# Performance work log

Measured on AMD Instinct MI355X. Metric: run time of the kernel, lower is better.

Reference implementation:

```python
import jax, jax.numpy as jnp
import numpy as np

D_MODEL = 1024
NUM_HEADS = 16
HEAD_DIM = D_MODEL // NUM_HEADS


def setup_inputs() -> dict:
    key = jax.random.key(0)
    k_x, k_wqkv, k_bqkv, k_wfc, k_bfc = jax.random.split(key, 5)
    scale_in = 1.0 / np.sqrt(D_MODEL)
    return {
        "x": jax.random.normal(k_x, (2, 2048, D_MODEL), dtype=jnp.float32),
        # torch nn.Linear stores weight as [out_features, in_features]
        "w_qkv": jax.random.uniform(k_wqkv, (3 * D_MODEL, D_MODEL), jnp.float32, -scale_in, scale_in),
        "b_qkv": jax.random.uniform(k_bqkv, (3 * D_MODEL,), jnp.float32, -scale_in, scale_in),
        "w_fc": jax.random.uniform(k_wfc, (D_MODEL, D_MODEL), jnp.float32, -scale_in, scale_in),
        "b_fc": jax.random.uniform(k_bfc, (D_MODEL,), jnp.float32, -scale_in, scale_in),
    }


def reference(x, w_qkv, b_qkv, w_fc, b_fc):
    B, S, _ = x.shape
    # fused QKV projection: [B,S,3*d_model]
    qkv = jnp.einsum("bsd,ed->bse", x, w_qkv) + b_qkv
    # [B,S,H,3*head_dim] -> [B,H,S,3*head_dim]
    qkv = qkv.reshape(B, S, NUM_HEADS, 3 * HEAD_DIM).transpose(0, 2, 1, 3)
    Q, K, V = jnp.split(qkv, 3, axis=-1)  # each [B,H,S,head_dim]
    scores = jnp.einsum("bhqd,bhkd->bhqk", Q, K) / np.sqrt(HEAD_DIM).astype(np.float32)
    attention = jax.nn.softmax(scores, axis=-1)  # [B,H,S,S]
    values = jnp.einsum("bhqk,bhkd->bhqd", attention, V)
    # [B,H,S,head_dim] -> [B,S,d_model]
    values = values.transpose(0, 2, 1, 3).reshape(B, S, D_MODEL)
    out = jnp.einsum("bsd,ed->bse", values, w_fc) + b_fc
    return out
```

## Files before the change

kernel.cpp:

```cpp
#include <hip/hip_runtime.h>
#include <hip/hip_bf16.h>

#define D_MODEL 1024
#define NH 16
#define HD 64
#define BATCH 2
#define SEQ 2048

typedef __attribute__((ext_vector_type(8))) short short8;
typedef __attribute__((ext_vector_type(4))) float floatx4;

static __device__ __forceinline__ short f2bf(float f) {
    __hip_bfloat16 h = __float2bfloat16(f);
    return *reinterpret_cast<short*>(&h);
}

__global__ __launch_bounds__(256) void cvt_all(
    const float* __restrict__ x, const float* __restrict__ wq,
    const float* __restrict__ wf,
    short* __restrict__ Xb, short* __restrict__ Wqb, short* __restrict__ Wfb)
{
    int i = blockIdx.x * 256 + threadIdx.x;
    const float* src; short* dst; int off;
    if (i < 524288)      { src = x;  dst = Xb;  off = i; }
    else if (i < 917504) { src = wq; dst = Wqb; off = i - 524288; }
    else                 { src = wf; dst = Wfb; off = i - 917504; }
    float4 a = *reinterpret_cast<const float4*>(src + off * 8);
    float4 b = *reinterpret_cast<const float4*>(src + off * 8 + 4);
    short8 o;
    o[0] = f2bf(a.x); o[1] = f2bf(a.y); o[2] = f2bf(a.z); o[3] = f2bf(a.w);
    o[4] = f2bf(b.x); o[5] = f2bf(b.y); o[6] = f2bf(b.z); o[7] = f2bf(b.w);
    *reinterpret_cast<short8*>(dst + off * 8) = o;
}

__global__ __launch_bounds__(256) void qkv_gemm(
    const short* __restrict__ X, const short* __restrict__ W,
    const float* __restrict__ bias,
    short* __restrict__ Qs, short* __restrict__ Ks, short* __restrict__ Vt_g)
{
    __shared__ __align__(16) short As[128][72];
    __shared__ __align__(16) short Bs[128][72];
    const int tid = threadIdx.x;
    const int m0 = blockIdx.y * 128;
    const int n0 = blockIdx.x * 128;
    const int w = tid >> 6, lane = tid & 63;
    const int quad = lane >> 4, l15 = lane & 15;
    const int wm = (w >> 1) * 64, wn = (w & 1) * 64;

    floatx4 acc[4][4];
#pragma unroll
    for (int i = 0; i < 4; i++)
#pragma unroll
        for (int j = 0; j < 4; j++) acc[i][j] = (floatx4)0.0f;

    for (int k0 = 0; k0 < 1024; k0 += 64) {
        __syncthreads();
#pragma unroll
        for (int i = 0; i < 4; i++) {
            int c = tid + i * 256;
            int row = c >> 3, ck = c & 7;
            *reinterpret_cast<uint4*>(&As[row][ck * 8]) =
                *reinterpret_cast<const uint4*>(&X[(m0 + row) * 1024 + k0 + ck * 8]);
            *reinterpret_cast<uint4*>(&Bs[row][ck * 8]) =
                *reinterpret_cast<const uint4*>(&W[(n0 + row) * 1024 + k0 + ck * 8]);
        }
        __syncthreads();
#pragma unroll
        for (int kk = 0; kk < 2; kk++) {
            short8 a[4], b[4];
#pragma unroll
            for (int t = 0; t < 4; t++) {
                a[t] = *reinterpret_cast<const short8*>(&As[wm + t * 16 + l15][kk * 32 + quad * 8]);
                b[t] = *reinterpret_cast<const short8*>(&Bs[wn + t * 16 + l15][kk * 32 + quad * 8]);
            }
#pragma unroll
            for (int mt = 0; mt < 4; mt++)
#pragma unroll
                for (int nt = 0; nt < 4; nt++)
                    acc[mt][nt] = __builtin_amdgcn_mfma_f32_16x16x32_bf16(
                        a[mt], b[nt], acc[mt][nt], 0, 0, 0);
        }
    }

#pragma unroll
    for (int nt = 0; nt < 4; nt++) {
        int col = n0 + wn + nt * 16 + l15;
        float bv = bias[col];
        int h = col / 192;
        int j = col - h * 192;
#pragma unroll
        for (int mt = 0; mt < 4; mt++) {
#pragma unroll
            for (int r = 0; r < 4; r++) {
                int row = m0 + wm + mt * 16 + quad * 4 + r;
                float v = acc[mt][nt][r] + bv;
                int bi = row >> 11, s = row & 2047;
                int bh = bi * NH + h;
                if (j < 64)       Qs[(bh * SEQ + s) * HD + j] = f2bf(v * 0.125f);
                else if (j < 128) Ks[(bh * SEQ + s) * HD + (j - 64)] = f2bf(v);
                else              Vt_g[(bh * HD + (j - 128)) * SEQ + s] = f2bf(v);
            }
        }
    }
}

__global__ __launch_bounds__(256) void attn_kernel(
    const short* __restrict__ Qs, const short* __restrict__ Ks,
    const short* __restrict__ Vt_g, short* __restrict__ attn)
{
    __shared__ __align__(16) char smem[2 * 64 * 72 * 2];
    __shared__ __align__(16) short Pl[4][32][40];
    __shared__ float Ls[64];

    short (*Kl)[72] = (short(*)[72])smem;
    short (*Vt)[72] = (short(*)[72])(smem + 64 * 72 * 2);
    float (*Osum)[66] = (float(*)[66])smem;

    const int tid = threadIdx.x;
    const int w = tid >> 6, lane = tid & 63;
    const int wq = w >> 1, wk = w & 1;
    const int quad = lane >> 4, l15 = lane & 15;
    const int q0 = blockIdx.x * 64;
    const int h = blockIdx.y, bi = blockIdx.z;
    const int bh = bi * NH + h;
    const int kbase = bh * SEQ * HD;
    const int vbase = bh * HD * SEQ;

    short8 aq[2][2];
#pragma unroll
    for (int mt = 0; mt < 2; mt++) {
        const short* qp = Qs + kbase + (q0 + wq * 32 + mt * 16 + l15) * HD;
#pragma unroll
        for (int c = 0; c < 2; c++)
            aq[mt][c] = *reinterpret_cast<const short8*>(qp + c * 32 + quad * 8);
    }

    float l_acc[2][4];
    floatx4 o[2][4];
#pragma unroll
    for (int mt = 0; mt < 2; mt++) {
#pragma unroll
        for (int r = 0; r < 4; r++) l_acc[mt][r] = 0.f;
#pragma unroll
        for (int nt = 0; nt < 4; nt++) o[mt][nt] = (floatx4)0.0f;
    }

    for (int kt = 0; kt < SEQ; kt += 64) {
        __syncthreads();
#pragma unroll
        for (int i = 0; i < 2; i++) {
            int c = tid + i * 256;
            int row = c >> 3, ck = c & 7;
            *reinterpret_cast<uint4*>(&Kl[row][ck * 8]) =
                *reinterpret_cast<const uint4*>(&Ks[kbase + (kt + row) * HD + ck * 8]);
            *reinterpret_cast<uint4*>(&Vt[row][ck * 8]) =
                *reinterpret_cast<const uint4*>(&Vt_g[vbase + row * SEQ + kt + ck * 8]);
        }
        __syncthreads();

        floatx4 sf[2][2];
#pragma unroll
        for (int mt = 0; mt < 2; mt++)
#pragma unroll
            for (int nt = 0; nt < 2; nt++) sf[mt][nt] = (floatx4)0.0f;
#pragma unroll
        for (int c = 0; c < 2; c++) {
#pragma unroll
            for (int nt = 0; nt < 2; nt++) {
                short8 bk = *reinterpret_cast<const short8*>(
                    &Kl[wk * 32 + nt * 16 + l15][c * 32 + quad * 8]);
#pragma unroll
                for (int mt = 0; mt < 2; mt++)
                    sf[mt][nt] = __builtin_amdgcn_mfma_f32_16x16x32_bf16(
                        aq[mt][c], bk, sf[mt][nt], 0, 0, 0);
            }
        }

#pragma unroll
        for (int mt = 0; mt < 2; mt++) {
#pragma unroll
            for (int nt = 0; nt < 2; nt++) {
#pragma unroll
                for (int r = 0; r < 4; r++) {
                    float e = __expf(sf[mt][nt][r]);
                    l_acc[mt][r] += e;
                    Pl[w][mt * 16 + quad * 4 + r][nt * 16 + l15] = f2bf(e);
                }
            }
        }
        asm volatile("s_waitcnt lgkmcnt(0)" ::: "memory");

#pragma unroll
        for (int mt = 0; mt < 2; mt++) {
            short8 ap = *reinterpret_cast<const short8*>(&Pl[w][mt * 16 + l15][quad * 8]);
#pragma unroll
            for (int nt = 0; nt < 4; nt++) {
                short8 bv = *reinterpret_cast<const short8*>(
                    &Vt[nt * 16 + l15][wk * 32 + quad * 8]);
                o[mt][nt] = __builtin_amdgcn_mfma_f32_16x16x32_bf16(
                    ap, bv, o[mt][nt], 0, 0, 0);
            }
        }
    }

#pragma unroll
    for (int mt = 0; mt < 2; mt++)
#pragma unroll
        for (int r = 0; r < 4; r++)
#pragma unroll
            for (int mask = 1; mask < 16; mask <<= 1)
                l_acc[mt][r] += __shfl_xor(l_acc[mt][r], mask);

    __syncthreads();
    if (wk == 0) {
#pragma unroll
        for (int mt = 0; mt < 2; mt++) {
#pragma unroll
            for (int nt = 0; nt < 4; nt++)
#pragma unroll
                for (int r = 0; r < 4; r++)
                    Osum[wq * 32 + mt * 16 + quad * 4 + r][nt * 16 + l15] = o[mt][nt][r];
            if (l15 == 0)
#pragma unroll
                for (int r = 0; r < 4; r++)
                    Ls[wq * 32 + mt * 16 + quad * 4 + r] = l_acc[mt][r];
        }
    }
    __syncthreads();
    if (wk == 1) {
#pragma unroll
        for (int mt = 0; mt < 2; mt++) {
#pragma unroll
            for (int r = 0; r < 4; r++) {
                int qrow = wq * 32 + mt * 16 + quad * 4 + r;
                float lt = Ls[qrow] + l_acc[mt][r];
#pragma unroll
                for (int nt = 0; nt < 4; nt++) {
                    float val = (o[mt][nt][r] + Osum[qrow][nt * 16 + l15]) / lt;
                    attn[(bi * SEQ + q0 + qrow) * D_MODEL + h * HD + nt * 16 + l15] = f2bf(val);
                }
            }
        }
    }
}

__global__ __launch_bounds__(256) void fc_gemm(
    const short* __restrict__ A, const short* __restrict__ W,
    const float* __restrict__ bias, float* __restrict__ out)
{
    __shared__ __align__(16) short As[128][72];
    __shared__ __align__(16) short Bs[128][72];
    const int tid = threadIdx.x;
    const int m0 = blockIdx.y * 128;
    const int n0 = blockIdx.x * 128;
    const int w = tid >> 6, lane = tid & 63;
    const int quad = lane >> 4, l15 = lane & 15;
    const int wm = (w >> 1) * 64, wn = (w & 1) * 64;

    floatx4 acc[4][4];
#pragma unroll
    for (int i = 0; i < 4; i++)
#pragma unroll
        for (int j = 0; j < 4; j++) acc[i][j] = (floatx4)0.0f;

    for (int k0 = 0; k0 < 1024; k0 += 64) {
        __syncthreads();
#pragma unroll
        for (int i = 0; i < 4; i++) {
            int c = tid + i * 256;
            int row = c >> 3, ck = c & 7;
            *reinterpret_cast<uint4*>(&As[row][ck * 8]) =
                *reinterpret_cast<const uint4*>(&A[(m0 + row) * 1024 + k0 + ck * 8]);
            *reinterpret_cast<uint4*>(&Bs[row][ck * 8]) =
                *reinterpret_cast<const uint4*>(&W[(n0 + row) * 1024 + k0 + ck * 8]);
        }
        __syncthreads();
#pragma unroll
        for (int kk = 0; kk < 2; kk++) {
            short8 a[4], b[4];
#pragma unroll
            for (int t = 0; t < 4; t++) {
                a[t] = *reinterpret_cast<const short8*>(&As[wm + t * 16 + l15][kk * 32 + quad * 8]);
                b[t] = *reinterpret_cast<const short8*>(&Bs[wn + t * 16 + l15][kk * 32 + quad * 8]);
            }
#pragma unroll
            for (int mt = 0; mt < 4; mt++)
#pragma unroll
                for (int nt = 0; nt < 4; nt++)
                    acc[mt][nt] = __builtin_amdgcn_mfma_f32_16x16x32_bf16(
                        a[mt], b[nt], acc[mt][nt], 0, 0, 0);
        }
    }

#pragma unroll
    for (int nt = 0; nt < 4; nt++) {
        int col = n0 + wn + nt * 16 + l15;
        float bv = bias[col];
#pragma unroll
        for (int mt = 0; mt < 4; mt++) {
#pragma unroll
            for (int r = 0; r < 4; r++) {
                int row = m0 + wm + mt * 16 + quad * 4 + r;
                out[row * 1024 + col] = acc[mt][nt][r] + bv;
            }
        }
    }
}

extern "C" void kernel_launch(void* const* d_in, const int* in_sizes, int n_in,
                              void* d_out, int out_size, void* d_ws, size_t ws_size,
                              hipStream_t stream) {
    const float* x     = (const float*)d_in[0];
    const float* w_qkv = (const float*)d_in[1];
    const float* b_qkv = (const float*)d_in[2];
    const float* w_fc  = (const float*)d_in[3];
    const float* b_fc  = (const float*)d_in[4];
    float* out = (float*)d_out;

    const size_t M4 = 4u * 1024 * 1024;
    short* Xb    = (short*)d_ws;
    short* Wqb   = Xb + M4;
    short* Wfb   = Wqb + 3u * 1024 * 1024;
    short* Qs    = Wfb + 1024 * 1024;
    short* Ks    = Qs + M4;
    short* Vt_g  = Ks + M4;
    short* attnb = Xb;

    cvt_all<<<4096, 256, 0, stream>>>(x, w_qkv, w_fc, Xb, Wqb, Wfb);
    qkv_gemm<<<dim3(24, 32), 256, 0, stream>>>(Xb, Wqb, b_qkv, Qs, Ks, Vt_g);
    attn_kernel<<<dim3(32, 16, 2), 256, 0, stream>>>(Qs, Ks, Vt_g, attnb);
    fc_gemm<<<dim3(8, 32), 256, 0, stream>>>(attnb, Wfb, b_fc, out);
}
```

Before: 227.8 us.

## Stage QKV epilogue through LDS for coalesced stores; transpose score MFMA for packed P writes

The QKV GEMM now uses 128x64 tiles, so each block covers exactly one Q, K or V slice of one head. Its epilogue writes the tile into shared memory, transposing it for V, and then emits coalesced 16-byte global stores instead of scattered 2-byte ones. In attention, the QK^T MFMA operands are swapped so each lane holds four consecutive keys of one query. This lets P be written as packed bf16 pairs and cuts the row-sum shuffle reduction. The price is a smaller GEMM tile with less reuse, twice as many blocks, and an extra LDS round trip.

```diff
diff --git a/kernel.cpp b/kernel.cpp
--- a/kernel.cpp
+++ b/kernel.cpp
@@ -13,6 +13,11 @@
 static __device__ __forceinline__ short f2bf(float f) {
     __hip_bfloat16 h = __float2bfloat16(f);
     return *reinterpret_cast<short*>(&h);
+}
+static __device__ __forceinline__ unsigned int pk2bf(float a, float b) {
+    float2 t; t.x = a; t.y = b;
+    __hip_bfloat162 h2 = __float22bfloat162_rn(t);
+    return *reinterpret_cast<unsigned int*>(&h2);
 }
 
 __global__ __launch_bounds__(256) void cvt_all(
@@ -39,19 +44,23 @@
     short* __restrict__ Qs, short* __restrict__ Ks, short* __restrict__ Vt_g)
 {
     __shared__ __align__(16) short As[128][72];
-    __shared__ __align__(16) short Bs[128][72];
+    __shared__ __align__(16) short Bs[64][72];
     const int tid = threadIdx.x;
+    const int bx = blockIdx.x;
     const int m0 = blockIdx.y * 128;
-    const int n0 = blockIdx.x * 128;
+    const int n0 = bx * 64;
+    const int h = bx / 3, t = bx % 3;
+    const int bi = m0 >> 11;
+    const int sl0 = m0 & 2047;
     const int w = tid >> 6, lane = tid & 63;
     const int quad = lane >> 4, l15 = lane & 15;
-    const int wm = (w >> 1) * 64, wn = (w & 1) * 64;
-
-    floatx4 acc[4][4];
+    const int wm2 = w >> 1, wn2 = w & 1;
+
+    floatx4 acc[4][2];
 #pragma unroll
     for (int i = 0; i < 4; i++)
 #pragma unroll
-        for (int j = 0; j < 4; j++) acc[i][j] = (floatx4)0.0f;
+        for (int j = 0; j < 2; j++) acc[i][j] = (floatx4)0.0f;
 
     for (int k0 = 0; k0 < 1024; k0 += 64) {
         __syncthreads();
@@ -61,45 +70,71 @@
             int row = c >> 3, ck = c & 7;
             *reinterpret_cast<uint4*>(&As[row][ck * 8]) =
                 *reinterpret_cast<const uint4*>(&X[(m0 + row) * 1024 + k0 + ck * 8]);
+        }
+#pragma unroll
+        for (int i = 0; i < 2; i++) {
+            int c = tid + i * 256;
+            int row = c >> 3, ck = c & 7;
             *reinterpret_cast<uint4*>(&Bs[row][ck * 8]) =
                 *reinterpret_cast<const uint4*>(&W[(n0 + row) * 1024 + k0 + ck * 8]);
         }
         __syncthreads();
 #pragma unroll
         for (int kk = 0; kk < 2; kk++) {
-            short8 a[4], b[4];
-#pragma unroll
-            for (int t = 0; t < 4; t++) {
-                a[t] = *reinterpret_cast<const short8*>(&As[wm + t * 16 + l15][kk * 32 + quad * 8]);
-                b[t] = *reinterpret_cast<const short8*>(&Bs[wn + t * 16 + l15][kk * 32 + quad * 8]);
-            }
+            short8 a[4], b[2];
+#pragma unroll
+            for (int i = 0; i < 4; i++)
+                a[i] = *reinterpret_cast<const short8*>(&As[wm2 * 64 + i * 16 + l15][kk * 32 + quad * 8]);
+#pragma unroll
+            for (int j = 0; j < 2; j++)
+                b[j] = *reinterpret_cast<const short8*>(&Bs[wn2 * 32 + j * 16 + l15][kk * 32 + quad * 8]);
 #pragma unroll
             for (int mt = 0; mt < 4; mt++)
 #pragma unroll
-                for (int nt = 0; nt < 4; nt++)
+                for (int nt = 0; nt < 2; nt++)
                     acc[mt][nt] = __builtin_amdgcn_mfma_f32_16x16x32_bf16(
                         a[mt], b[nt], acc[mt][nt], 0, 0, 0);
         }
     }
 
-#pragma unroll
-    for (int nt = 0; nt < 4; nt++) {
-        int col = n0 + wn + nt * 16 + l15;
-        float bv = bias[col];
-        int h = col / 192;
-        int j = col - h * 192;
+    __syncthreads();
+    short* T = &As[0][0];
+#pragma unroll
+    for (int nt = 0; nt < 2; nt++) {
+        int col = wn2 * 32 + nt * 16 + l15;
+        float bv = bias[h * 192 + t * 64 + col];
 #pragma unroll
         for (int mt = 0; mt < 4; mt++) {
 #pragma unroll
             for (int r = 0; r < 4; r++) {
-                int row = m0 + wm + mt * 16 + quad * 4 + r;
+                int ml = wm2 * 64 + mt * 16 + quad * 4 + r;
                 float v = acc[mt][nt][r] + bv;
-                int bi = row >> 11, s = row & 2047;
-                int bh = bi * NH + h;
-                if (j < 64)       Qs[(bh * SEQ + s) * HD + j] = f2bf(v * 0.125f);
-                else if (j < 128) Ks[(bh * SEQ + s) * HD + (j - 64)] = f2bf(v);
-                else              Vt_g[(bh * HD + (j - 128)) * SEQ + s] = f2bf(v);
-            }
+                if (t == 0) v *= 0.125f;
+                if (t < 2) As[ml][col] = f2bf(v);
+                else       T[col * 136 + ml] = f2bf(v);
+            }
+        }
+    }
+    __syncthreads();
+
+    if (t < 2) {
+        short* dst = (t == 0) ? Qs : Ks;
+#pragma unroll
+        for (int i = 0; i < 4; i++) {
+            int c = tid + i * 256;
+            int row = c >> 3, ck = c & 7;
+            uint4 u = *reinterpret_cast<const uint4*>(&As[row][ck * 8]);
+            *reinterpret_cast<uint4*>(
+                &dst[((size_t)(bi * NH + h) * SEQ + sl0 + row) * HD + ck * 8]) = u;
+        }
+    } else {
+#pragma unroll
+        for (int i = 0; i < 4; i++) {
+            int c = tid + i * 256;
+            int drow = c >> 4, ck = c & 15;
+            uint4 u = *reinterpret_cast<const uint4*>(&T[drow * 136 + ck * 8]);
+            *reinterpret_cast<uint4*>(
+                &Vt_g[((size_t)(bi * NH + h) * HD + drow) * SEQ + sl0 + ck * 8]) = u;
         }
     }
 }
@@ -108,9 +143,9 @@
     const short* __restrict__ Qs, const short* __restrict__ Ks,
     const short* __restrict__ Vt_g, short* __restrict__ attn)
 {
-    __shared__ __align__(16) char smem[2 * 64 * 72 * 2];
+    __shared__ __align__(16) char smem[64 * 72 * 2 * 2];
     __shared__ __align__(16) short Pl[4][32][40];
-    __shared__ float Ls[64];
+    __shared__ float Ls[2][64];
 
     short (*Kl)[72] = (short(*)[72])smem;
     short (*Vt)[72] = (short(*)[72])(smem + 64 * 72 * 2);
@@ -128,22 +163,19 @@
 
     short8 aq[2][2];
 #pragma unroll
-    for (int mt = 0; mt < 2; mt++) {
-        const short* qp = Qs + kbase + (q0 + wq * 32 + mt * 16 + l15) * HD;
+    for (int qt2 = 0; qt2 < 2; qt2++) {
+        const short* qp = Qs + kbase + (q0 + wq * 32 + qt2 * 16 + l15) * HD;
 #pragma unroll
         for (int c = 0; c < 2; c++)
-            aq[mt][c] = *reinterpret_cast<const short8*>(qp + c * 32 + quad * 8);
-    }
-
-    float l_acc[2][4];
+            aq[qt2][c] = *reinterpret_cast<const short8*>(qp + c * 32 + quad * 8);
+    }
+
+    float l_acc[2] = {0.f, 0.f};
     floatx4 o[2][4];
 #pragma unroll
-    for (int mt = 0; mt < 2; mt++) {
-#pragma unroll
-        for (int r = 0; r < 4; r++) l_acc[mt][r] = 0.f;
+    for (int mt = 0; mt < 2; mt++)
 #pragma unroll
         for (int nt = 0; nt < 4; nt++) o[mt][nt] = (floatx4)0.0f;
-    }
 
     for (int kt = 0; kt < SEQ; kt += 64) {
         __syncthreads();
@@ -160,32 +192,35 @@
 
         floatx4 sf[2][2];
 #pragma unroll
-        for (int mt = 0; mt < 2; mt++)
-#pragma unroll
-            for (int nt = 0; nt < 2; nt++) sf[mt][nt] = (floatx4)0.0f;
+        for (int kt2 = 0; kt2 < 2; kt2++)
+#pragma unroll
+            for (int qt2 = 0; qt2 < 2; qt2++) sf[kt2][qt2] = (floatx4)0.0f;
 #pragma unroll
         for (int c = 0; c < 2; c++) {
 #pragma unroll
-            for (int nt = 0; nt < 2; nt++) {
+            for (int kt2 = 0; kt2 < 2; kt2++) {
                 short8 bk = *reinterpret_cast<const short8*>(
-                    &Kl[wk * 32 + nt * 16 + l15][c * 32 + quad * 8]);
-#pragma unroll
-                for (int mt = 0; mt < 2; mt++)
-                    sf[mt][nt] = __builtin_amdgcn_mfma_f32_16x16x32_bf16(
-                        aq[mt][c], bk, sf[mt][nt], 0, 0, 0);
-            }
-        }
-
-#pragma unroll
-        for (int mt = 0; mt < 2; mt++) {
-#pragma unroll
-            for (int nt = 0; nt < 2; nt++) {
-#pragma unroll
-                for (int r = 0; r < 4; r++) {
-                    float e = __expf(sf[mt][nt][r]);
-                    l_acc[mt][r] += e;
-                    Pl[w][mt * 16 + quad * 4 + r][nt * 16 + l15] = f2bf(e);
-                }
+                    &Kl[wk * 32 + kt2 * 16 + l15][c * 32 + quad * 8]);
+#pragma unroll
+                for (int qt2 = 0; qt2 < 2; qt2++)
+                    sf[kt2][qt2] = __builtin_amdgcn_mfma_f32_16x16x32_bf16(
+                        bk, aq[qt2][c], sf[kt2][qt2], 0, 0, 0);
+            }
+        }
+
+#pragma unroll
+        for (int kt2 = 0; kt2 < 2; kt2++) {
+#pragma unroll
+            for (int qt2 = 0; qt2 < 2; qt2++) {
+                float e0 = __expf(sf[kt2][qt2][0]);
+                float e1 = __expf(sf[kt2][qt2][1]);
+                float e2 = __expf(sf[kt2][qt2][2]);
+                float e3 = __expf(sf[kt2][qt2][3]);
+                l_acc[qt2] += (e0 + e1) + (e2 + e3);
+                uint2 p;
+                p.x = pk2bf(e0, e1);
+                p.y = pk2bf(e2, e3);
+                *reinterpret_cast<uint2*>(&Pl[w][qt2 * 16 + l15][kt2 * 16 + quad * 4]) = p;
             }
         }
         asm volatile("s_waitcnt lgkmcnt(0)" ::: "memory");
@@ -204,27 +239,24 @@
     }
 
 #pragma unroll
-    for (int mt = 0; mt < 2; mt++)
-#pragma unroll
-        for (int r = 0; r < 4; r++)
-#pragma unroll
-            for (int mask = 1; mask < 16; mask <<= 1)
-                l_acc[mt][r] += __shfl_xor(l_acc[mt][r], mask);
-
+    for (int qt2 = 0; qt2 < 2; qt2++) {
+        l_acc[qt2] += __shfl_xor(l_acc[qt2], 16);
+        l_acc[qt2] += __shfl_xor(l_acc[qt2], 32);
+    }
+    if (quad == 0) {
+        Ls[wk][wq * 32 + l15]      = l_acc[0];
+        Ls[wk][wq * 32 + 16 + l15] = l_acc[1];
+    }
     __syncthreads();
+
     if (wk == 0) {
 #pragma unroll
-        for (int mt = 0; mt < 2; mt++) {
+        for (int mt = 0; mt < 2; mt++)
 #pragma unroll
             for (int nt = 0; nt < 4; nt++)
 #pragma unroll
                 for (int r = 0; r < 4; r++)
                     Osum[wq * 32 + mt * 16 + quad * 4 + r][nt * 16 + l15] = o[mt][nt][r];
-            if (l15 == 0)
-#pragma unroll
-                for (int r = 0; r < 4; r++)
-                    Ls[wq * 32 + mt * 16 + quad * 4 + r] = l_acc[mt][r];
-        }
     }
     __syncthreads();
     if (wk == 1) {
@@ -233,7 +265,7 @@
 #pragma unroll
             for (int r = 0; r < 4; r++) {
                 int qrow = wq * 32 + mt * 16 + quad * 4 + r;
-                float lt = Ls[qrow] + l_acc[mt][r];
+                float lt = Ls[0][qrow] + Ls[1][qrow];
 #pragma unroll
                 for (int nt = 0; nt < 4; nt++) {
                     float val = (o[mt][nt][r] + Osum[qrow][nt * 16 + l15]) / lt;
@@ -327,7 +359,7 @@
     short* attnb = Xb;
 
     cvt_all<<<4096, 256, 0, stream>>>(x, w_qkv, w_fc, Xb, Wqb, Wfb);
-    qkv_gemm<<<dim3(24, 32), 256, 0, stream>>>(Xb, Wqb, b_qkv, Qs, Ks, Vt_g);
+    qkv_gemm<<<dim3(48, 32), 256, 0, stream>>>(Xb, Wqb, b_qkv, Qs, Ks, Vt_g);
     attn_kernel<<<dim3(32, 16, 2), 256, 0, stream>>>(Qs, Ks, Vt_g, attnb);
     fc_gemm<<<dim3(8, 32), 256, 0, stream>>>(attnb, Wfb, b_fc, out);
 }
```

New measurement: 224.7 us. No clear change (-1.3%).
